# Optimization experiments

Measured on AMD Instinct MI355X. Metric: run time of the kernel, lower is better.

The kernel has to match this reference:

```python
import jax, jax.numpy as jnp
import numpy as np

N_NODES = 100000
N_EDGES = 1600000
F_IN, H1, H2 = 128, 64, 32


def spmm(src, dst, edge_weight, x, n_nodes):
    # A @ x with A in COO form: out[dst] += w * x[src]
    msgs = x[src] * edge_weight[:, None]          # [E, d] gather + scale
    return jax.ops.segment_sum(msgs, dst, num_segments=n_nodes)


def setup_inputs() -> dict:
    key = jax.random.key(0)
    k1, k2, k3, k4, k5, k6 = jax.random.split(key, 6)
    features = jax.random.normal(k1, (N_NODES, F_IN), dtype=jnp.float32)
    # positive weights, roughly 1/deg scale as in a normalized adjacency
    edge_weight = jax.random.uniform(k2, (N_EDGES,), dtype=jnp.float32) * 0.125
    W1 = jax.random.normal(k3, (F_IN, H1), dtype=jnp.float32) * (1.0 / np.sqrt(F_IN))
    W2 = jax.random.normal(k4, (H1, H2), dtype=jnp.float32) * (1.0 / np.sqrt(H1))
    src = jax.random.randint(k5, (N_EDGES,), 0, N_NODES, dtype=jnp.int64 if jax.config.jax_enable_x64 else jnp.int32)
    dst = jax.random.randint(k6, (N_EDGES,), 0, N_NODES, dtype=jnp.int64 if jax.config.jax_enable_x64 else jnp.int32)
    return {"features": features, "edge_weight": edge_weight, "W1": W1, "W2": W2,
            "src": src, "dst": dst}


def reference(features, edge_weight, W1, W2, src, dst):
    # Layer 1: relu(A @ (X W1)); dropout is identity (eval mode / rate 0)
    h1 = jax.nn.relu(spmm(src, dst, edge_weight, features @ W1, N_NODES))  # [N, H1]
    # Layer 2: A @ (h1 W2)
    embeddings = spmm(src, dst, edge_weight, h1 @ W2, N_NODES)             # [N, H2]
    return embeddings
```

## Files before the change

### kernel.cpp

```cpp
#include <hip/hip_runtime.h>
#include <hip/hip_fp16.h>


constexpr int N_NODES = 100000;
constexpr int N_EDGES = 1600000;
constexpr int F_IN = 128;
constexpr int H1 = 64;
constexpr int H2 = 32;
constexpr int BSHIFT = 9;
constexpr int BNODES = 1 << BSHIFT;
constexpr int NBUCK = (N_NODES + BNODES - 1) / BNODES;
constexpr int CAP = 10240;
constexpr int CHUNK = 4096;
constexpr int P1_WGS = (N_EDGES + CHUNK - 1) / CHUNK;
constexpr int GEMM_WGS = (N_NODES + 255) / 256;

__global__ __launch_bounds__(256) void init_cursors(int* __restrict__ cursor)
{
    int t = threadIdx.x;
    if (t < NBUCK) cursor[t] = t * CAP;
}

__global__ __launch_bounds__(256) void pass1_bin_gemm1(
    const int* __restrict__ src, const int* __restrict__ dst,
    const float* __restrict__ w, int* __restrict__ cursor,
    int2* __restrict__ staging,
    const float* __restrict__ X, const float* __restrict__ W1,
    __half* __restrict__ xw1out)
{
    __shared__ float smem[F_IN * H1];

    if (blockIdx.x < GEMM_WGS) {
        for (int i = threadIdx.x; i < F_IN * H1; i += 256) smem[i] = W1[i];
        __syncthreads();
        int row = blockIdx.x * 256 + threadIdx.x;
        if (row >= N_NODES) return;
        const float4* xr = reinterpret_cast<const float4*>(X + (size_t)row * F_IN);
        float4 acc[H1 / 4];
#pragma unroll
        for (int j = 0; j < H1 / 4; ++j) acc[j] = make_float4(0.f, 0.f, 0.f, 0.f);
        for (int k4 = 0; k4 < F_IN / 4; ++k4) {
            float4 xv = xr[k4];
#pragma unroll
            for (int kk = 0; kk < 4; ++kk) {
                float xk = (kk == 0) ? xv.x : (kk == 1) ? xv.y
                         : (kk == 2) ? xv.z : xv.w;
                const float4* wr = reinterpret_cast<const float4*>(
                    &smem[(k4 * 4 + kk) * H1]);
#pragma unroll
                for (int j = 0; j < H1 / 4; ++j) {
                    float4 wv = wr[j];
                    acc[j].x += xk * wv.x;
                    acc[j].y += xk * wv.y;
                    acc[j].z += xk * wv.z;
                    acc[j].w += xk * wv.w;
                }
            }
        }
        __half2* oh = reinterpret_cast<__half2*>(xw1out + (size_t)row * H1);
#pragma unroll
        for (int j = 0; j < H1 / 4; ++j) {
            oh[j * 2 + 0] = __floats2half2_rn(acc[j].x, acc[j].y);
            oh[j * 2 + 1] = __floats2half2_rn(acc[j].z, acc[j].w);
        }
        return;
    }

    int* lcnt  = (int*)smem;
    int* lbase = lcnt + 256;

    int e0 = (blockIdx.x - GEMM_WGS) * CHUNK;
    int nhere = N_EDGES - e0; if (nhere > CHUNK) nhere = CHUNK;

    lcnt[threadIdx.x] = 0;
    __syncthreads();

    int   es[16];
    int   ed[16];
    float ew[16];
    {
        bool v = (threadIdx.x * 16) < nhere;
        int tb = e0 + threadIdx.x * 16;
        if (v) {
            const int4* sp = reinterpret_cast<const int4*>(src + tb);
            const int4* dp = reinterpret_cast<const int4*>(dst + tb);
            const float4* wp = reinterpret_cast<const float4*>(w + tb);
#pragma unroll
            for (int q = 0; q < 4; ++q) {
                int4 sv = sp[q], dv = dp[q]; float4 wv = wp[q];
                es[4*q+0]=sv.x; es[4*q+1]=sv.y; es[4*q+2]=sv.z; es[4*q+3]=sv.w;
                ed[4*q+0]=dv.x; ed[4*q+1]=dv.y; ed[4*q+2]=dv.z; ed[4*q+3]=dv.w;
                ew[4*q+0]=wv.x; ew[4*q+1]=wv.y; ew[4*q+2]=wv.z; ew[4*q+3]=wv.w;
            }
        } else {
#pragma unroll
            for (int k = 0; k < 16; ++k) { es[k]=0; ed[k]=-1; ew[k]=0.f; }
        }
    }
#pragma unroll
    for (int k = 0; k < 16; ++k)
        if (ed[k] >= 0) atomicAdd(&lcnt[ed[k] >> BSHIFT], 1);
    __syncthreads();
    if (threadIdx.x < NBUCK) {
        int c = lcnt[threadIdx.x];
        lbase[threadIdx.x] = (c > 0) ? atomicAdd(&cursor[threadIdx.x], c) : 0;
    }
    __syncthreads();
    lcnt[threadIdx.x] = 0;
    __syncthreads();
#pragma unroll
    for (int k = 0; k < 16; ++k) {
        if (ed[k] >= 0) {
            int b = ed[k] >> BSHIFT;
            int r = atomicAdd(&lcnt[b], 1);
            int pos = lbase[b] + r;
            if (pos < (b + 1) * CAP)
                staging[pos] = make_int2(
                    es[k] | ((ed[k] & (BNODES - 1)) << 17),
                    __float_as_int(ew[k]));
        }
    }
}

__global__ __launch_bounds__(1024) void sort_bucket(
    const int* __restrict__ cursor, const int2* __restrict__ staging,
    int2* __restrict__ csr, int2* __restrict__ seg)
{
    __shared__ int  lcnt[BNODES];
    __shared__ int  lofs[BNODES];
    __shared__ int2 sorted[CAP];

    int b = blockIdx.x, t = threadIdx.x;
    int base = b * CAP;
    int cnt = cursor[b] - base; if (cnt > CAP) cnt = CAP;

    if (t < BNODES) lcnt[t] = 0;
    __syncthreads();

    for (int j = t; j < cnt; j += 1024)
        atomicAdd(&lcnt[(staging[base + j].x >> 17) & (BNODES - 1)], 1);
    __syncthreads();

    int v = (t < BNODES) ? lcnt[t] : 0;
    if (t < BNODES) lofs[t] = v;
    __syncthreads();
    for (int off = 1; off < BNODES; off <<= 1) {
        int add = (t >= off && t < BNODES) ? lofs[t - off] : 0;
        __syncthreads();
        if (t < BNODES) lofs[t] += add;
        __syncthreads();
    }
    if (t < BNODES) {
        int excl = lofs[t] - v;
        seg[b * BNODES + t] = make_int2(base + excl, v);
        lcnt[t] = excl;
    }
    __syncthreads();

    for (int j = t; j < cnt; j += 1024) {
        int2 c = staging[base + j];
        int node = (c.x >> 17) & (BNODES - 1);
        int pos = atomicAdd(&lcnt[node], 1);
        sorted[pos] = make_int2(c.x & 0x1FFFF, c.y);
    }
    __syncthreads();

    for (int j = t; j < cnt; j += 1024) csr[base + j] = sorted[j];
}

__global__ __launch_bounds__(256) void spmm1_fused(
    const int2* __restrict__ seg, const int2* __restrict__ csr,
    const __half* __restrict__ xin, const float* __restrict__ W2,
    __half* __restrict__ h1w2h)
{
    int gid = blockIdx.x * 256 + threadIdx.x;
    int node = gid >> 6;
    int f = gid & 63;
    int par = f >> 5;
    int f2 = f & 31;

    float w2r[32];
#pragma unroll
    for (int kk = 0; kk < 32; ++kk)
        w2r[kk] = W2[(par * 32 + kk) * H2 + f2];

    int2 s = seg[node];
    int end = s.x + s.y;
    float2 a0 = make_float2(0.f, 0.f), a1 = make_float2(0.f, 0.f);
    float2 a2 = make_float2(0.f, 0.f), a3 = make_float2(0.f, 0.f);
    int e = s.x + par;
    for (; e + 6 < end; e += 8) {
        int2 c0 = csr[e], c1 = csr[e + 2], c2 = csr[e + 4], c3 = csr[e + 6];
        float2 x0 = __half22float2(
            *reinterpret_cast<const __half2*>(&xin[(size_t)c0.x * H1 + 2 * f2]));
        float2 x1 = __half22float2(
            *reinterpret_cast<const __half2*>(&xin[(size_t)c1.x * H1 + 2 * f2]));
        float2 x2 = __half22float2(
            *reinterpret_cast<const __half2*>(&xin[(size_t)c2.x * H1 + 2 * f2]));
        float2 x3 = __half22float2(
            *reinterpret_cast<const __half2*>(&xin[(size_t)c3.x * H1 + 2 * f2]));
        float w0 = __int_as_float(c0.y), w1 = __int_as_float(c1.y);
        float w2v = __int_as_float(c2.y), w3 = __int_as_float(c3.y);
        a0.x += w0 * x0.x; a0.y += w0 * x0.y;
        a1.x += w1 * x1.x; a1.y += w1 * x1.y;
        a2.x += w2v * x2.x; a2.y += w2v * x2.y;
        a3.x += w3 * x3.x; a3.y += w3 * x3.y;
    }
    for (; e < end; e += 2) {
        int2 c = csr[e];
        float2 x = __half22float2(
            *reinterpret_cast<const __half2*>(&xin[(size_t)c.x * H1 + 2 * f2]));
        float wv = __int_as_float(c.y);
        a0.x += wv * x.x; a0.y += wv * x.y;
    }
    float rx = (a0.x + a1.x) + (a2.x + a3.x);
    float ry = (a0.y + a1.y) + (a2.y + a3.y);
    rx += __shfl_xor(rx, 32, 64);
    ry += __shfl_xor(ry, 32, 64);
    rx = fmaxf(rx, 0.f); ry = fmaxf(ry, 0.f);

    float o = 0.f;
#pragma unroll
    for (int kk = 0; kk < 32; kk += 2) {
        int p = 16 * par + (kk >> 1);
        o += __shfl(rx, p, 64) * w2r[kk];
        o += __shfl(ry, p, 64) * w2r[kk + 1];
    }
    o += __shfl_xor(o, 32, 64);
    if (f < 32)
        h1w2h[(size_t)node * H2 + f2] = __float2half(o);
}

__global__ __launch_bounds__(256) void spmm_csr32h(
    const int2* __restrict__ seg, const int2* __restrict__ csr,
    const __half* __restrict__ xin, float* __restrict__ out)
{
    int gid = blockIdx.x * 256 + threadIdx.x;
    int node = gid >> 6;
    int lane = gid & 63;
    int slot = lane >> 4;
    int f2 = lane & 15;

    int2 s = seg[node];
    int end = s.x + s.y;
    float2 a0 = make_float2(0.f, 0.f), a1 = make_float2(0.f, 0.f);
    float2 a2 = make_float2(0.f, 0.f), a3 = make_float2(0.f, 0.f);
    int e = s.x + slot;
    for (; e + 12 < end; e += 16) {
        int2 c0 = csr[e], c1 = csr[e + 4], c2 = csr[e + 8], c3 = csr[e + 12];
        float2 x0 = __half22float2(
            *reinterpret_cast<const __half2*>(&xin[(size_t)c0.x * H2 + 2 * f2]));
        float2 x1 = __half22float2(
            *reinterpret_cast<const __half2*>(&xin[(size_t)c1.x * H2 + 2 * f2]));
        float2 x2 = __half22float2(
            *reinterpret_cast<const __half2*>(&xin[(size_t)c2.x * H2 + 2 * f2]));
        float2 x3 = __half22float2(
            *reinterpret_cast<const __half2*>(&xin[(size_t)c3.x * H2 + 2 * f2]));
        float w0 = __int_as_float(c0.y), w1 = __int_as_float(c1.y);
        float w2v = __int_as_float(c2.y), w3 = __int_as_float(c3.y);
        a0.x += w0 * x0.x; a0.y += w0 * x0.y;
        a1.x += w1 * x1.x; a1.y += w1 * x1.y;
        a2.x += w2v * x2.x; a2.y += w2v * x2.y;
        a3.x += w3 * x3.x; a3.y += w3 * x3.y;
    }
    for (; e < end; e += 4) {
        int2 c = csr[e];
        float2 x = __half22float2(
            *reinterpret_cast<const __half2*>(&xin[(size_t)c.x * H2 + 2 * f2]));
        float wv = __int_as_float(c.y);
        a0.x += wv * x.x; a0.y += wv * x.y;
    }
    float ox = (a0.x + a1.x) + (a2.x + a3.x);
    float oy = (a0.y + a1.y) + (a2.y + a3.y);
    ox += __shfl_xor(ox, 16, 64); oy += __shfl_xor(oy, 16, 64);
    ox += __shfl_xor(ox, 32, 64); oy += __shfl_xor(oy, 32, 64);
    if (lane < 16)
        *reinterpret_cast<float2*>(&out[(size_t)node * H2 + 2 * f2]) =
            make_float2(ox, oy);
}

extern "C" void kernel_launch(void* const* d_in, const int* in_sizes, int n_in,
                              void* d_out, int out_size, void* d_ws, size_t ws_size,
                              hipStream_t stream)
{
    const float* features    = (const float*)d_in[0];
    const float* edge_weight = (const float*)d_in[1];
    const float* W1          = (const float*)d_in[2];
    const float* W2          = (const float*)d_in[3];
    const int*   src         = (const int*)d_in[4];
    const int*   dst         = (const int*)d_in[5];
    float* out = (float*)d_out;

    char* p = (char*)d_ws;
    __half* xw1h   = (__half*)p;    p += (size_t)N_NODES * H1 * 2;
    __half* h1w2h  = (__half*)p;    p += (size_t)N_NODES * H2 * 2;
    int2*  staging = (int2*)p;      p += (size_t)NBUCK * CAP * 8;
    int2*  csr     = (int2*)p;      p += (size_t)NBUCK * CAP * 8;
    int2*  seg     = (int2*)p;      p += (size_t)NBUCK * BNODES * 8;
    int*   cursor  = (int*)p;       p += 256 * 4;

    init_cursors<<<1, 256, 0, stream>>>(cursor);
    pass1_bin_gemm1<<<P1_WGS + GEMM_WGS, 256, 0, stream>>>(
        src, dst, edge_weight, cursor, staging, features, W1, xw1h);
    sort_bucket<<<NBUCK, 1024, 0, stream>>>(cursor, staging, csr, seg);

    spmm1_fused<<<(N_NODES * 64) / 256, 256, 0, stream>>>(seg, csr, xw1h, W2, h1w2h);
    spmm_csr32h<<<(N_NODES * 64) / 256, 256, 0, stream>>>(seg, csr, h1w2h, out);
}
```

Before: 180.4 us.

## Pad CSR segments to multiples of four and use wave-uniform vectorized edge loads

The bucket sort now pads each node's edge segment to a multiple of four with zero-weight dummy edges, so the SpMM kernels can read the CSR with aligned 16-byte int4 loads and loop without scalar tails. Segment start and count are made wave-uniform with readfirstlane, which lets the loop control and CSR address math live in scalar registers. The goal is fewer, wider index loads and less divergent remainder handling. In exchange, padding adds wasted gathers of row 0, and buckets with many high-degree nodes may overflow CAP sooner, which would silently drop edges.

```diff
diff --git a/kernel.cpp b/kernel.cpp
--- a/kernel.cpp
+++ b/kernel.cpp
@@ -129,6 +129,7 @@
     __shared__ int  lcnt[BNODES];
     __shared__ int  lofs[BNODES];
     __shared__ int2 sorted[CAP];
+    __shared__ int  total_sh;
 
     int b = blockIdx.x, t = threadIdx.x;
     int base = b * CAP;
@@ -142,7 +143,8 @@
     __syncthreads();
 
     int v = (t < BNODES) ? lcnt[t] : 0;
-    if (t < BNODES) lofs[t] = v;
+    int pc = (v + 3) & ~3;
+    if (t < BNODES) lofs[t] = pc;
     __syncthreads();
     for (int off = 1; off < BNODES; off <<= 1) {
         int add = (t >= off && t < BNODES) ? lofs[t - off] : 0;
@@ -151,9 +153,15 @@
         __syncthreads();
     }
     if (t < BNODES) {
-        int excl = lofs[t] - v;
-        seg[b * BNODES + t] = make_int2(base + excl, v);
-        lcnt[t] = excl;
+        int pexcl = lofs[t] - pc;
+        seg[b * BNODES + t] = make_int2(base + pexcl, pc);
+        lcnt[t] = pexcl;
+        for (int j = v; j < pc; ++j)
+            if (pexcl + j < CAP) sorted[pexcl + j] = make_int2(0, 0);
+        if (t == BNODES - 1) {
+            int tot = lofs[t]; if (tot > CAP) tot = CAP;
+            total_sh = tot;
+        }
     }
     __syncthreads();
 
@@ -161,11 +169,12 @@
         int2 c = staging[base + j];
         int node = (c.x >> 17) & (BNODES - 1);
         int pos = atomicAdd(&lcnt[node], 1);
-        sorted[pos] = make_int2(c.x & 0x1FFFF, c.y);
-    }
-    __syncthreads();
-
-    for (int j = t; j < cnt; j += 1024) csr[base + j] = sorted[j];
+        if (pos < CAP) sorted[pos] = make_int2(c.x & 0x1FFFF, c.y);
+    }
+    __syncthreads();
+
+    int total = total_sh;
+    for (int j = t; j < total; j += 1024) csr[base + j] = sorted[j];
 }
 
 __global__ __launch_bounds__(256) void spmm1_fused(
@@ -174,7 +183,7 @@
     __half* __restrict__ h1w2h)
 {
     int gid = blockIdx.x * 256 + threadIdx.x;
-    int node = gid >> 6;
+    int node = __builtin_amdgcn_readfirstlane(gid >> 6);
     int f = gid & 63;
     int par = f >> 5;
     int f2 = f & 31;
@@ -185,36 +194,26 @@
         w2r[kk] = W2[(par * 32 + kk) * H2 + f2];
 
     int2 s = seg[node];
-    int end = s.x + s.y;
+    int start = __builtin_amdgcn_readfirstlane(s.x);
+    int cntp  = __builtin_amdgcn_readfirstlane(s.y);
+    const int4* csr4 = reinterpret_cast<const int4*>(csr);
+
     float2 a0 = make_float2(0.f, 0.f), a1 = make_float2(0.f, 0.f);
-    float2 a2 = make_float2(0.f, 0.f), a3 = make_float2(0.f, 0.f);
-    int e = s.x + par;
-    for (; e + 6 < end; e += 8) {
-        int2 c0 = csr[e], c1 = csr[e + 2], c2 = csr[e + 4], c3 = csr[e + 6];
-        float2 x0 = __half22float2(
-            *reinterpret_cast<const __half2*>(&xin[(size_t)c0.x * H1 + 2 * f2]));
-        float2 x1 = __half22float2(
-            *reinterpret_cast<const __half2*>(&xin[(size_t)c1.x * H1 + 2 * f2]));
-        float2 x2 = __half22float2(
-            *reinterpret_cast<const __half2*>(&xin[(size_t)c2.x * H1 + 2 * f2]));
-        float2 x3 = __half22float2(
-            *reinterpret_cast<const __half2*>(&xin[(size_t)c3.x * H1 + 2 * f2]));
-        float w0 = __int_as_float(c0.y), w1 = __int_as_float(c1.y);
-        float w2v = __int_as_float(c2.y), w3 = __int_as_float(c3.y);
-        a0.x += w0 * x0.x; a0.y += w0 * x0.y;
-        a1.x += w1 * x1.x; a1.y += w1 * x1.y;
-        a2.x += w2v * x2.x; a2.y += w2v * x2.y;
-        a3.x += w3 * x3.x; a3.y += w3 * x3.y;
-    }
-    for (; e < end; e += 2) {
-        int2 c = csr[e];
-        float2 x = __half22float2(
-            *reinterpret_cast<const __half2*>(&xin[(size_t)c.x * H1 + 2 * f2]));
-        float wv = __int_as_float(c.y);
-        a0.x += wv * x.x; a0.y += wv * x.y;
-    }
-    float rx = (a0.x + a1.x) + (a2.x + a3.x);
-    float ry = (a0.y + a1.y) + (a2.y + a3.y);
+    for (int e = start; e < start + cntp; e += 4) {
+        int4 p0 = csr4[(e >> 1) + 0];
+        int4 p1 = csr4[(e >> 1) + 1];
+        int  sA = par ? p0.z : p0.x;
+        float wA = __int_as_float(par ? p0.w : p0.y);
+        int  sB = par ? p1.z : p1.x;
+        float wB = __int_as_float(par ? p1.w : p1.y);
+        float2 xA = __half22float2(
+            *reinterpret_cast<const __half2*>(&xin[(size_t)sA * H1 + 2 * f2]));
+        float2 xB = __half22float2(
+            *reinterpret_cast<const __half2*>(&xin[(size_t)sB * H1 + 2 * f2]));
+        a0.x += wA * xA.x; a0.y += wA * xA.y;
+        a1.x += wB * xB.x; a1.y += wB * xB.y;
+    }
+    float rx = a0.x + a1.x, ry = a0.y + a1.y;
     rx += __shfl_xor(rx, 32, 64);
     ry += __shfl_xor(ry, 32, 64);
     rx = fmaxf(rx, 0.f); ry = fmaxf(ry, 0.f);
@@ -236,42 +235,48 @@
     const __half* __restrict__ xin, float* __restrict__ out)
 {
     int gid = blockIdx.x * 256 + threadIdx.x;
-    int node = gid >> 6;
+    int node = __builtin_amdgcn_readfirstlane(gid >> 6);
     int lane = gid & 63;
     int slot = lane >> 4;
     int f2 = lane & 15;
 
     int2 s = seg[node];
-    int end = s.x + s.y;
+    int start = __builtin_amdgcn_readfirstlane(s.x);
+    int cntp  = __builtin_amdgcn_readfirstlane(s.y);
+    int endp = start + cntp;
+    const int4* csr4 = reinterpret_cast<const int4*>(csr);
+
     float2 a0 = make_float2(0.f, 0.f), a1 = make_float2(0.f, 0.f);
-    float2 a2 = make_float2(0.f, 0.f), a3 = make_float2(0.f, 0.f);
-    int e = s.x + slot;
-    for (; e + 12 < end; e += 16) {
-        int2 c0 = csr[e], c1 = csr[e + 4], c2 = csr[e + 8], c3 = csr[e + 12];
-        float2 x0 = __half22float2(
-            *reinterpret_cast<const __half2*>(&xin[(size_t)c0.x * H2 + 2 * f2]));
-        float2 x1 = __half22float2(
-            *reinterpret_cast<const __half2*>(&xin[(size_t)c1.x * H2 + 2 * f2]));
-        float2 x2 = __half22float2(
-            *reinterpret_cast<const __half2*>(&xin[(size_t)c2.x * H2 + 2 * f2]));
-        float2 x3 = __half22float2(
-            *reinterpret_cast<const __half2*>(&xin[(size_t)c3.x * H2 + 2 * f2]));
-        float w0 = __int_as_float(c0.y), w1 = __int_as_float(c1.y);
-        float w2v = __int_as_float(c2.y), w3 = __int_as_float(c3.y);
-        a0.x += w0 * x0.x; a0.y += w0 * x0.y;
-        a1.x += w1 * x1.x; a1.y += w1 * x1.y;
-        a2.x += w2v * x2.x; a2.y += w2v * x2.y;
-        a3.x += w3 * x3.x; a3.y += w3 * x3.y;
-    }
-    for (; e < end; e += 4) {
-        int2 c = csr[e];
-        float2 x = __half22float2(
-            *reinterpret_cast<const __half2*>(&xin[(size_t)c.x * H2 + 2 * f2]));
-        float wv = __int_as_float(c.y);
-        a0.x += wv * x.x; a0.y += wv * x.y;
-    }
-    float ox = (a0.x + a1.x) + (a2.x + a3.x);
-    float oy = (a0.y + a1.y) + (a2.y + a3.y);
+    int e = start;
+    for (; e + 8 <= endp; e += 8) {
+        int4 q0 = csr4[(e >> 1) + 0];
+        int4 q1 = csr4[(e >> 1) + 1];
+        int4 q2 = csr4[(e >> 1) + 2];
+        int4 q3 = csr4[(e >> 1) + 3];
+        int4 qa = (slot & 2) ? q1 : q0;
+        int  sA = (slot & 1) ? qa.z : qa.x;
+        float wA = __int_as_float((slot & 1) ? qa.w : qa.y);
+        int4 qb = (slot & 2) ? q3 : q2;
+        int  sB = (slot & 1) ? qb.z : qb.x;
+        float wB = __int_as_float((slot & 1) ? qb.w : qb.y);
+        float2 xA = __half22float2(
+            *reinterpret_cast<const __half2*>(&xin[(size_t)sA * H2 + 2 * f2]));
+        float2 xB = __half22float2(
+            *reinterpret_cast<const __half2*>(&xin[(size_t)sB * H2 + 2 * f2]));
+        a0.x += wA * xA.x; a0.y += wA * xA.y;
+        a1.x += wB * xB.x; a1.y += wB * xB.y;
+    }
+    if (e < endp) {
+        int4 q0 = csr4[(e >> 1) + 0];
+        int4 q1 = csr4[(e >> 1) + 1];
+        int4 qa = (slot & 2) ? q1 : q0;
+        int  sA = (slot & 1) ? qa.z : qa.x;
+        float wA = __int_as_float((slot & 1) ? qa.w : qa.y);
+        float2 xA = __half22float2(
+            *reinterpret_cast<const __half2*>(&xin[(size_t)sA * H2 + 2 * f2]));
+        a0.x += wA * xA.x; a0.y += wA * xA.y;
+    }
+    float ox = a0.x + a1.x, oy = a0.y + a1.y;
     ox += __shfl_xor(ox, 16, 64); oy += __shfl_xor(oy, 16, 64);
     ox += __shfl_xor(ox, 32, 64); oy += __shfl_xor(oy, 32, 64);
     if (lane < 16)
```

New measurement: 158.0 us. 1.14x faster.
